# Optimization experiments

Measured on AMD Instinct MI355X. Metric: run time of the kernel, lower is better.

Reference implementation:

```python
import jax, jax.numpy as jnp
import numpy as np

N = 50000       # nodes
E = 800000      # directed edges (before self-loops)
IN = 128        # in_channels
H = 8           # heads
C = 32          # hidden_channels (per head)
OUT = 4         # out_channels
NS_ATT = 0.2    # PyG GATConv attention leaky-relu slope
NS_ACT = 0.01   # model activation leaky-relu slope
EPS = 1e-5      # BatchNorm eps


def setup_inputs() -> dict:
    key = jax.random.key(0)
    ks = jax.random.split(key, 18)
    s = 0.05
    return {
        "x": jax.random.normal(ks[0], (N, IN), jnp.float32),
        "edge_index": jax.random.randint(ks[1], (2, E), 0, N, dtype=jnp.int32),
        # layer 1: GATConv(IN -> C, heads=H, concat)
        "W1": jax.random.normal(ks[2], (IN, H * C), jnp.float32) * s,
        "as1": jax.random.normal(ks[3], (H, C), jnp.float32) * s,
        "ad1": jax.random.normal(ks[4], (H, C), jnp.float32) * s,
        "b1": jnp.zeros((H * C,), jnp.float32),
        "g1": jnp.ones((H * C,), jnp.float32),
        "be1": jnp.zeros((H * C,), jnp.float32),
        # middle layer: GATConv(H*C -> C, heads=H, concat) + BN + residual
        "W2": jax.random.normal(ks[5], (H * C, H * C), jnp.float32) * s,
        "as2": jax.random.normal(ks[6], (H, C), jnp.float32) * s,
        "ad2": jax.random.normal(ks[7], (H, C), jnp.float32) * s,
        "b2": jnp.zeros((H * C,), jnp.float32),
        "g2": jnp.ones((H * C,), jnp.float32),
        "be2": jnp.zeros((H * C,), jnp.float32),
        # final layer: GATConv(H*C -> OUT, heads=1, concat=False)
        "W3": jax.random.normal(ks[8], (H * C, OUT), jnp.float32) * s,
        "as3": jax.random.normal(ks[9], (1, OUT), jnp.float32) * s,
        "ad3": jax.random.normal(ks[10], (1, OUT), jnp.float32) * s,
        "b3": jnp.zeros((OUT,), jnp.float32),
    }


def _lrelu(x, slope):
    return jnp.where(x >= 0, x, slope * x)


def _gat_conv(x, src, dst, W, a_src, a_dst, bias, heads, ch, concat):
    # PyG GATConv: h = x @ W per head; edge logit = LReLU(a_src.h_j + a_dst.h_i)
    n = x.shape[0]
    h = (x @ W).reshape(n, heads, ch)                      # [N,H,C]
    al_s = jnp.sum(h * a_src, axis=-1)                     # [N,H]
    al_d = jnp.sum(h * a_dst, axis=-1)                     # [N,H]
    logits = _lrelu(al_s[src] + al_d[dst], NS_ATT)         # [E,H]
    # segment softmax over edges grouped by destination node
    m = jax.ops.segment_max(logits, dst, num_segments=n)   # [N,H]
    e = jnp.exp(logits - m[dst])
    denom = jax.ops.segment_sum(e, dst, num_segments=n)
    alpha = e / (denom[dst] + 1e-16)                       # [E,H]
    out = jax.ops.segment_sum(alpha[:, :, None] * h[src], dst, num_segments=n)  # [N,H,C]
    if concat:
        return out.reshape(n, heads * ch) + bias
    return out.mean(axis=1) + bias


def _bn(x, gamma, beta):
    mu = jnp.mean(x, axis=0)
    var = jnp.mean((x - mu) ** 2, axis=0)
    return (x - mu) * jax.lax.rsqrt(var + EPS) * gamma + beta


def reference(x, edge_index, W1, as1, ad1, b1, g1, be1,
              W2, as2, ad2, b2, g2, be2, W3, as3, ad3, b3):
    n = x.shape[0]
    loops = jnp.arange(n, dtype=edge_index.dtype)          # self-loops (PyG default)
    src = jnp.concatenate([edge_index[0], loops])
    dst = jnp.concatenate([edge_index[1], loops])
    h = _lrelu(_bn(_gat_conv(x, src, dst, W1, as1, ad1, b1, H, C, True), g1, be1), NS_ACT)
    residual = h
    h = _lrelu(_bn(_gat_conv(h, src, dst, W2, as2, ad2, b2, H, C, True), g2, be2), NS_ACT)
    h = h + residual
    return _gat_conv(h, src, dst, W3, as3, ad3, b3, 1, OUT, False)
```

## Files before the change

### kernel.cpp

```cpp
#include <hip/hip_runtime.h>

typedef __attribute__((ext_vector_type(8))) short bf16x8;
typedef __attribute__((ext_vector_type(4))) float f32x4;

__device__ __forceinline__ float lrelu(float x, float s) { return x >= 0.f ? x : s * x; }
__device__ __forceinline__ float b2f(unsigned short u) {
  union { unsigned int i; float f; } v; v.i = ((unsigned int)u) << 16; return v.f;
}
__device__ __forceinline__ float b2f_lo(unsigned int u) {
  union { unsigned int i; float f; } v; v.i = u << 16; return v.f;
}
__device__ __forceinline__ float b2f_hi(unsigned int u) {
  union { unsigned int i; float f; } v; v.i = u & 0xffff0000u; return v.f;
}
__device__ __forceinline__ unsigned short f2b(float f) {
  union { float f; unsigned int i; } v; v.f = f;
  unsigned int r = v.i + 0x7fffu + ((v.i >> 16) & 1u);
  return (unsigned short)(r >> 16);
}

__global__ __launch_bounds__(256) void k_hist(const int* __restrict__ dst, int e,
                                              int* __restrict__ cnt) {
  int i = blockIdx.x * 256 + threadIdx.x;
  if (i < e) atomicAdd(&cnt[dst[i]], 1);
}

__global__ __launch_bounds__(256) void k_bsum(const int* __restrict__ cnt,
                                              int* __restrict__ bsum, int n) {
  const int base = blockIdx.x * 1024;
  const int t = threadIdx.x;
  int s = 0;
#pragma unroll
  for (int i = 0; i < 4; ++i) {
    int idx = base + t + i * 256;
    if (idx < n) s += cnt[idx] + 1;
  }
#pragma unroll
  for (int off = 1; off < 64; off <<= 1) s += __shfl_xor(s, off);
  __shared__ int ws[4];
  const int lane = t & 63, w = t >> 6;
  if (lane == 0) ws[w] = s;
  __syncthreads();
  if (t == 0) bsum[blockIdx.x] = ws[0] + ws[1] + ws[2] + ws[3];
}

__global__ __launch_bounds__(64) void k_scanb(const int* __restrict__ bsum,
                                              int* __restrict__ boff,
                                              int* __restrict__ ptrN, int B) {
  const int lane = threadIdx.x;
  int v = lane < B ? bsum[lane] : 0;
  int incl = v;
#pragma unroll
  for (int off = 1; off < 64; off <<= 1) {
    int u = __shfl_up(incl, off);
    if (lane >= off) incl += u;
  }
  if (lane < B) boff[lane] = incl - v;
  if (lane == 63) *ptrN = incl;
}

__global__ __launch_bounds__(256) void k_scanl(const int* __restrict__ cnt,
                                               const int* __restrict__ boff,
                                               int* __restrict__ ptr,
                                               int* __restrict__ fill, int n) {
  __shared__ int ws[4];
  const int t = threadIdx.x;
  const int base = blockIdx.x * 1024 + t * 4;
  int v0 = base + 0 < n ? cnt[base + 0] + 1 : 0;
  int v1 = base + 1 < n ? cnt[base + 1] + 1 : 0;
  int v2 = base + 2 < n ? cnt[base + 2] + 1 : 0;
  int v3 = base + 3 < n ? cnt[base + 3] + 1 : 0;
  const int tsum = v0 + v1 + v2 + v3;
  const int lane = t & 63, w = t >> 6;
  int incl = tsum;
#pragma unroll
  for (int off = 1; off < 64; off <<= 1) {
    int u = __shfl_up(incl, off);
    if (lane >= off) incl += u;
  }
  if (lane == 63) ws[w] = incl;
  __syncthreads();
  int excl = boff[blockIdx.x] + incl - tsum;
  for (int i = 0; i < w; ++i) excl += ws[i];
  if (base + 0 < n) { ptr[base + 0] = excl; fill[base + 0] = excl; }
  excl += v0;
  if (base + 1 < n) { ptr[base + 1] = excl; fill[base + 1] = excl; }
  excl += v1;
  if (base + 2 < n) { ptr[base + 2] = excl; fill[base + 2] = excl; }
  excl += v2;
  if (base + 3 < n) { ptr[base + 3] = excl; fill[base + 3] = excl; }
}

__global__ __launch_bounds__(256) void k_scatter(const int* __restrict__ srce,
                                                 const int* __restrict__ dste,
                                                 int e, int n,
                                                 int* __restrict__ fill,
                                                 int* __restrict__ srcs) {
  int i = blockIdx.x * 256 + threadIdx.x;
  if (i < e) {
    int pos = atomicAdd(&fill[dste[i]], 1);
    srcs[pos] = srce[i];
  } else if (i < e + n) {
    int v = i - e;
    int pos = atomicAdd(&fill[v], 1);
    srcs[pos] = v;
  }
}

__global__ __launch_bounds__(256) void k_prep(const float* __restrict__ x,
                                              unsigned short* __restrict__ xb,
                                              const float* __restrict__ W1,
                                              unsigned short* __restrict__ w1t,
                                              const float* __restrict__ W2,
                                              unsigned short* __restrict__ w2t, int n4) {
  int i = blockIdx.x * 256 + threadIdx.x;
  if (i < n4) {
    float4 v = ((const float4*)x)[i];
    ushort4 o;
    o.x = f2b(v.x); o.y = f2b(v.y); o.z = f2b(v.z); o.w = f2b(v.w);
    ((ushort4*)xb)[i] = o;
    return;
  }
  i -= n4;
  if (i < 256 * 128) {
    int nn = i / 128, k = i - nn * 128;
    w1t[i] = f2b(W1[(size_t)k * 256 + nn]);
    return;
  }
  i -= 256 * 128;
  if (i < 256 * 256) {
    int nn = i / 256, k = i - nn * 256;
    w2t[i] = f2b(W2[(size_t)k * 256 + nn]);
  }
}

__global__ __launch_bounds__(256) void k_mfma(const unsigned short* __restrict__ A,
                                              const unsigned short* __restrict__ BT,
                                              unsigned short* __restrict__ C,
                                              int M, int Nn, int K) {
  __shared__ unsigned int Asu[128 * 20];
  __shared__ unsigned int Bsu[128 * 20];
  const int tid = threadIdx.x;
  const int bm = blockIdx.x * 128, bn = blockIdx.y * 128;
  const int w = tid >> 6, lane = tid & 63;
  const int wm = w >> 1, wn = w & 1;
  const int l16 = lane & 15, lg = lane >> 4;
  f32x4 acc[4][4] = {};
  for (int k0 = 0; k0 < K; k0 += 32) {
#pragma unroll
    for (int rep = 0; rep < 2; ++rep) {
      int ci = tid + rep * 256;
      int row = ci >> 2, cg = ci & 3;
      int ar = bm + row;
      ar = ar < M ? ar : M - 1;
      uint4 av = *(const uint4*)(A + (size_t)ar * K + k0 + cg * 8);
      *(uint4*)&Asu[row * 20 + cg * 4] = av;
      uint4 bv = *(const uint4*)(BT + (size_t)(bn + row) * K + k0 + cg * 8);
      *(uint4*)&Bsu[row * 20 + cg * 4] = bv;
    }
    __syncthreads();
    bf16x8 aF[4], bF[4];
#pragma unroll
    for (int mi = 0; mi < 4; ++mi)
      aF[mi] = *(const bf16x8*)&Asu[(wm * 64 + mi * 16 + l16) * 20 + lg * 4];
#pragma unroll
    for (int ni = 0; ni < 4; ++ni)
      bF[ni] = *(const bf16x8*)&Bsu[(wn * 64 + ni * 16 + l16) * 20 + lg * 4];
#pragma unroll
    for (int mi = 0; mi < 4; ++mi)
#pragma unroll
      for (int ni = 0; ni < 4; ++ni)
        acc[mi][ni] =
            __builtin_amdgcn_mfma_f32_16x16x32_bf16(aF[mi], bF[ni], acc[mi][ni], 0, 0, 0);
    __syncthreads();
  }
#pragma unroll
  for (int mi = 0; mi < 4; ++mi) {
#pragma unroll
    for (int r = 0; r < 4; ++r) {
      int grow = bm + wm * 64 + mi * 16 + lg * 4 + r;
      if (grow < M) {
#pragma unroll
        for (int ni = 0; ni < 4; ++ni) {
          int gcol = bn + wn * 64 + ni * 16 + l16;
          C[(size_t)grow * Nn + gcol] = f2b(acc[mi][ni][r]);
        }
      }
    }
  }
}

__global__ __launch_bounds__(256) void k_attn(const unsigned short* __restrict__ h,
                                              const float* __restrict__ as_,
                                              const float* __restrict__ ad_,
                                              float* __restrict__ als,
                                              float* __restrict__ ald, int n) {
  int wid = (blockIdx.x * 256 + threadIdx.x) >> 6;
  int lane = threadIdx.x & 63;
  if (wid >= n) return;
  ushort4 hv = *(const ushort4*)(h + (size_t)wid * 256 + lane * 4);
  float hx = b2f(hv.x), hy = b2f(hv.y), hz = b2f(hv.z), hw = b2f(hv.w);
  float4 av = *(const float4*)(as_ + lane * 4);
  float4 dv = *(const float4*)(ad_ + lane * 4);
  float ps = hx * av.x + hy * av.y + hz * av.z + hw * av.w;
  float pd = hx * dv.x + hy * dv.y + hz * dv.z + hw * dv.w;
  ps += __shfl_xor(ps, 1); pd += __shfl_xor(pd, 1);
  ps += __shfl_xor(ps, 2); pd += __shfl_xor(pd, 2);
  ps += __shfl_xor(ps, 4); pd += __shfl_xor(pd, 4);
  if ((lane & 7) == 0) {
    als[(size_t)wid * 8 + (lane >> 3)] = ps;
    ald[(size_t)wid * 8 + (lane >> 3)] = pd;
  }
}

__global__ __launch_bounds__(256) void k_agg(const unsigned short* __restrict__ h,
                                             const float* __restrict__ als,
                                             const float* __restrict__ ald,
                                             const int* __restrict__ ptr,
                                             const int* __restrict__ srcs,
                                             const float* __restrict__ bias,
                                             unsigned short* __restrict__ out, int n) {
  int wid = (blockIdx.x * 256 + threadIdx.x) >> 6;
  int lane = threadIdx.x & 63;
  if (wid >= n) return;
  const int beg = ptr[wid], end = ptr[wid + 1];
  const int L = lane & 31;
  const int half = lane >> 5;
  const int hh = L >> 2;
  const float adh = ald[(size_t)wid * 8 + hh];
  float s = 0.f;
  float a0 = 0.f, a1 = 0.f, a2 = 0.f, a3 = 0.f, a4 = 0.f, a5 = 0.f, a6 = 0.f, a7 = 0.f;
  int j = beg + half;
  int sN = j < end ? srcs[j] : 0;
  for (; j < end; j += 2) {
    int nj = j + 2;
    int sNn = nj < end ? srcs[nj] : 0;
    float lg = lrelu(als[(size_t)sN * 8 + hh] + adh, 0.2f);
    float wt = __expf(lg);
    s += wt;
    uint4 hv = *(const uint4*)(h + (size_t)sN * 256 + L * 8);
    a0 += wt * b2f_lo(hv.x); a1 += wt * b2f_hi(hv.x);
    a2 += wt * b2f_lo(hv.y); a3 += wt * b2f_hi(hv.y);
    a4 += wt * b2f_lo(hv.z); a5 += wt * b2f_hi(hv.z);
    a6 += wt * b2f_lo(hv.w); a7 += wt * b2f_hi(hv.w);
    sN = sNn;
  }
  a0 += __shfl_xor(a0, 32); a1 += __shfl_xor(a1, 32);
  a2 += __shfl_xor(a2, 32); a3 += __shfl_xor(a3, 32);
  a4 += __shfl_xor(a4, 32); a5 += __shfl_xor(a5, 32);
  a6 += __shfl_xor(a6, 32); a7 += __shfl_xor(a7, 32);
  s += __shfl_xor(s, 32);
  s += __shfl_xor(s, 1);
  s += __shfl_xor(s, 2);
  s *= 0.25f;
  const float inv = 1.f / (s + 1e-16f);
  if (half == 0) {
    const float4* bp = (const float4*)(bias + L * 8);
    float4 bv0 = bp[0], bv1 = bp[1];
    float o0 = a0 * inv + bv0.x, o1 = a1 * inv + bv0.y;
    float o2 = a2 * inv + bv0.z, o3 = a3 * inv + bv0.w;
    float o4 = a4 * inv + bv1.x, o5 = a5 * inv + bv1.y;
    float o6 = a6 * inv + bv1.z, o7 = a7 * inv + bv1.w;
    uint4 ov;
    ov.x = (unsigned int)f2b(o0) | ((unsigned int)f2b(o1) << 16);
    ov.y = (unsigned int)f2b(o2) | ((unsigned int)f2b(o3) << 16);
    ov.z = (unsigned int)f2b(o4) | ((unsigned int)f2b(o5) << 16);
    ov.w = (unsigned int)f2b(o6) | ((unsigned int)f2b(o7) << 16);
    *(uint4*)(out + (size_t)wid * 256 + L * 8) = ov;
  }
}

__global__ __launch_bounds__(256) void k_bnp1(const unsigned short* __restrict__ x,
                                              float* __restrict__ partial, int n) {
  const int t = threadIdx.x;
  const int q = t & 63;
  const int rsub = t >> 6;
  float s0 = 0, s1 = 0, s2 = 0, s3 = 0, q0 = 0, q1 = 0, q2 = 0, q3 = 0;
  for (int r = blockIdx.x * 4 + rsub; r < n; r += 1024) {
    ushort4 v = *(const ushort4*)(x + (size_t)r * 256 + q * 4);
    float f0 = b2f(v.x), f1 = b2f(v.y), f2 = b2f(v.z), f3 = b2f(v.w);
    s0 += f0; s1 += f1; s2 += f2; s3 += f3;
    q0 += f0 * f0; q1 += f1 * f1; q2 += f2 * f2; q3 += f3 * f3;
  }
  __shared__ float ls[4][512];
  ls[rsub][q * 4 + 0] = s0; ls[rsub][q * 4 + 1] = s1;
  ls[rsub][q * 4 + 2] = s2; ls[rsub][q * 4 + 3] = s3;
  ls[rsub][256 + q * 4 + 0] = q0; ls[rsub][256 + q * 4 + 1] = q1;
  ls[rsub][256 + q * 4 + 2] = q2; ls[rsub][256 + q * 4 + 3] = q3;
  __syncthreads();
  float a = ls[0][t] + ls[1][t] + ls[2][t] + ls[3][t];
  float b = ls[0][256 + t] + ls[1][256 + t] + ls[2][256 + t] + ls[3][256 + t];
  partial[blockIdx.x * 512 + t] = a;
  partial[blockIdx.x * 512 + 256 + t] = b;
}

__global__ __launch_bounds__(256) void k_bnp2(const float* __restrict__ partial,
                                              float* __restrict__ statsOut) {
  const int idx = blockIdx.x * 256 + threadIdx.x;
  float s = 0.f;
  for (int b = 0; b < 256; ++b) s += partial[b * 512 + idx];
  statsOut[idx] = s;
}

__global__ __launch_bounds__(256) void k_bnact(const unsigned short* __restrict__ x,
                                               const float* __restrict__ stats,
                                               const float* __restrict__ ga,
                                               const float* __restrict__ be,
                                               unsigned short* __restrict__ out, int n) {
  const float invn = 1.f / (float)n;
  const int tot4 = n * 64;
  for (int t = blockIdx.x * 256 + threadIdx.x; t < tot4; t += gridDim.x * 256) {
    int i0 = t * 4;
    int c = i0 & 255;
    ushort4 xu = *(const ushort4*)(x + i0);
    float4 sm = *(const float4*)(stats + c);
    float4 sq = *(const float4*)(stats + 256 + c);
    float4 gv = *(const float4*)(ga + c);
    float4 bev = *(const float4*)(be + c);
    float o0, o1, o2, o3, mu, var, sc;
    mu = sm.x * invn; var = sq.x * invn - mu * mu; sc = gv.x * rsqrtf(var + 1e-5f);
    o0 = (b2f(xu.x) - mu) * sc + bev.x; o0 = o0 >= 0.f ? o0 : 0.01f * o0;
    mu = sm.y * invn; var = sq.y * invn - mu * mu; sc = gv.y * rsqrtf(var + 1e-5f);
    o1 = (b2f(xu.y) - mu) * sc + bev.y; o1 = o1 >= 0.f ? o1 : 0.01f * o1;
    mu = sm.z * invn; var = sq.z * invn - mu * mu; sc = gv.z * rsqrtf(var + 1e-5f);
    o2 = (b2f(xu.z) - mu) * sc + bev.z; o2 = o2 >= 0.f ? o2 : 0.01f * o2;
    mu = sm.w * invn; var = sq.w * invn - mu * mu; sc = gv.w * rsqrtf(var + 1e-5f);
    o3 = (b2f(xu.w) - mu) * sc + bev.w; o3 = o3 >= 0.f ? o3 : 0.01f * o3;
    ushort4 ob;
    ob.x = f2b(o0); ob.y = f2b(o1); ob.z = f2b(o2); ob.w = f2b(o3);
    *(ushort4*)(out + i0) = ob;
  }
}

__global__ __launch_bounds__(256) void k_bnact3(const unsigned short* __restrict__ x,
                                                const float* __restrict__ stats,
                                                const float* __restrict__ ga,
                                                const float* __restrict__ be,
                                                const unsigned short* __restrict__ res,
                                                const float* __restrict__ W3,
                                                const float* __restrict__ as3,
                                                const float* __restrict__ ad3,
                                                float* __restrict__ h3,
                                                float* __restrict__ als3,
                                                float* __restrict__ ald3, int n) {
  const float invn = 1.f / (float)n;
  int wid = (blockIdx.x * 256 + threadIdx.x) >> 6;
  int lane = threadIdx.x & 63;
  if (wid >= n) return;
  const int c = lane * 4;
  ushort4 xu = *(const ushort4*)(x + (size_t)wid * 256 + c);
  ushort4 rv = *(const ushort4*)(res + (size_t)wid * 256 + c);
  float4 sm = *(const float4*)(stats + c);
  float4 sq = *(const float4*)(stats + 256 + c);
  float4 gv = *(const float4*)(ga + c);
  float4 bev = *(const float4*)(be + c);
  float o0, o1, o2, o3, mu, var, sc;
  mu = sm.x * invn; var = sq.x * invn - mu * mu; sc = gv.x * rsqrtf(var + 1e-5f);
  o0 = (b2f(xu.x) - mu) * sc + bev.x; o0 = (o0 >= 0.f ? o0 : 0.01f * o0) + b2f(rv.x);
  mu = sm.y * invn; var = sq.y * invn - mu * mu; sc = gv.y * rsqrtf(var + 1e-5f);
  o1 = (b2f(xu.y) - mu) * sc + bev.y; o1 = (o1 >= 0.f ? o1 : 0.01f * o1) + b2f(rv.y);
  mu = sm.z * invn; var = sq.z * invn - mu * mu; sc = gv.z * rsqrtf(var + 1e-5f);
  o2 = (b2f(xu.z) - mu) * sc + bev.z; o2 = (o2 >= 0.f ? o2 : 0.01f * o2) + b2f(rv.z);
  mu = sm.w * invn; var = sq.w * invn - mu * mu; sc = gv.w * rsqrtf(var + 1e-5f);
  o3 = (b2f(xu.w) - mu) * sc + bev.w; o3 = (o3 >= 0.f ? o3 : 0.01f * o3) + b2f(rv.w);
  const float4* Wp = (const float4*)W3 + lane * 4;
  float4 w0 = Wp[0], w1 = Wp[1], w2 = Wp[2], w3 = Wp[3];
  float a0 = o0 * w0.x + o1 * w1.x + o2 * w2.x + o3 * w3.x;
  float a1 = o0 * w0.y + o1 * w1.y + o2 * w2.y + o3 * w3.y;
  float a2 = o0 * w0.z + o1 * w1.z + o2 * w2.z + o3 * w3.z;
  float a3 = o0 * w0.w + o1 * w1.w + o2 * w2.w + o3 * w3.w;
#pragma unroll
  for (int off = 1; off < 64; off <<= 1) {
    a0 += __shfl_xor(a0, off);
    a1 += __shfl_xor(a1, off);
    a2 += __shfl_xor(a2, off);
    a3 += __shfl_xor(a3, off);
  }
  if (lane == 0) {
    *(float4*)(h3 + (size_t)wid * 4) = make_float4(a0, a1, a2, a3);
    als3[wid] = a0 * as3[0] + a1 * as3[1] + a2 * as3[2] + a3 * as3[3];
    ald3[wid] = a0 * ad3[0] + a1 * ad3[1] + a2 * ad3[2] + a3 * ad3[3];
  }
}

__global__ __launch_bounds__(256) void k_agg3(const float* __restrict__ h3,
                                              const float* __restrict__ als3,
                                              const float* __restrict__ ald3,
                                              const int* __restrict__ ptr,
                                              const int* __restrict__ srcs,
                                              const float* __restrict__ b3,
                                              float* __restrict__ out, int n) {
  int wid = (blockIdx.x * 256 + threadIdx.x) >> 6;
  int lane = threadIdx.x & 63;
  if (wid >= n) return;
  const int beg = ptr[wid], end = ptr[wid + 1];
  const float aldh = ald3[wid];
  float s = 0.f, a0 = 0.f, a1 = 0.f, a2 = 0.f, a3 = 0.f;
  for (int j = beg + lane; j < end; j += 64) {
    int sN = srcs[j];
    float wgt = __expf(lrelu(als3[sN] + aldh, 0.2f));
    s += wgt;
    float4 hv = *(const float4*)(h3 + (size_t)sN * 4);
    a0 += wgt * hv.x;
    a1 += wgt * hv.y;
    a2 += wgt * hv.z;
    a3 += wgt * hv.w;
  }
#pragma unroll
  for (int off = 1; off < 64; off <<= 1) {
    s += __shfl_xor(s, off);
    a0 += __shfl_xor(a0, off);
    a1 += __shfl_xor(a1, off);
    a2 += __shfl_xor(a2, off);
    a3 += __shfl_xor(a3, off);
  }
  if (lane == 0) {
    float inv = 1.f / (s + 1e-16f);
    out[(size_t)wid * 4 + 0] = a0 * inv + b3[0];
    out[(size_t)wid * 4 + 1] = a1 * inv + b3[1];
    out[(size_t)wid * 4 + 2] = a2 * inv + b3[2];
    out[(size_t)wid * 4 + 3] = a3 * inv + b3[3];
  }
}

extern "C" void kernel_launch(void* const* d_in, const int* in_sizes, int n_in,
                              void* d_out, int out_size, void* d_ws, size_t ws_size,
                              hipStream_t stream) {
  const float* x   = (const float*)d_in[0];
  const int*   ei  = (const int*)d_in[1];
  const float* W1  = (const float*)d_in[2];
  const float* as1 = (const float*)d_in[3];
  const float* ad1 = (const float*)d_in[4];
  const float* b1  = (const float*)d_in[5];
  const float* ga1 = (const float*)d_in[6];
  const float* be1 = (const float*)d_in[7];
  const float* W2  = (const float*)d_in[8];
  const float* as2 = (const float*)d_in[9];
  const float* ad2 = (const float*)d_in[10];
  const float* b2  = (const float*)d_in[11];
  const float* ga2 = (const float*)d_in[12];
  const float* be2 = (const float*)d_in[13];
  const float* W3  = (const float*)d_in[14];
  const float* as3 = (const float*)d_in[15];
  const float* ad3 = (const float*)d_in[16];
  const float* b3  = (const float*)d_in[17];

  const int N = in_sizes[0] / 128;
  const int E = in_sizes[1] / 2;
  const int ET = E + N;
  float* out = (float*)d_out;

  char* w = (char*)d_ws;
  auto alloc = [&](size_t bytes) -> void* {
    void* p = (void*)w;
    w += (bytes + 255) & ~(size_t)255;
    return p;
  };
  int* ptr              = (int*)alloc((size_t)(N + 1) * 4);
  int* fill             = (int*)alloc((size_t)N * 4);
  int* cnt              = (int*)alloc((size_t)N * 4);
  int* bsum             = (int*)alloc(64 * 4);
  int* boff             = (int*)alloc(64 * 4);
  int* srcs             = (int*)alloc((size_t)ET * 4);
  unsigned short* hbuf  = (unsigned short*)alloc((size_t)N * 256 * 2);
  unsigned short* aggb  = (unsigned short*)alloc((size_t)N * 256 * 2);
  unsigned short* a1b   = (unsigned short*)alloc((size_t)N * 256 * 2);
  unsigned short* xb    = (unsigned short*)alloc((size_t)N * 128 * 2);
  unsigned short* w1t   = (unsigned short*)alloc(256 * 128 * 2);
  unsigned short* w2t   = (unsigned short*)alloc(256 * 256 * 2);
  float* als            = (float*)alloc((size_t)N * 8 * 4);
  float* ald            = (float*)alloc((size_t)N * 8 * 4);
  float* h3             = (float*)alloc((size_t)N * 4 * 4);
  float* als3           = (float*)alloc((size_t)N * 4);
  float* ald3           = (float*)alloc((size_t)N * 4);
  float* partial        = (float*)alloc(256 * 512 * 4);
  float* stats          = (float*)alloc(1024 * 4);

  const int* esrc = ei;
  const int* edst = ei + E;

  hipMemsetAsync(cnt, 0, (size_t)N * 4, stream);

  const int B = (N + 1023) / 1024;
  k_hist<<<(E + 255) / 256, 256, 0, stream>>>(edst, E, cnt);
  k_bsum<<<B, 256, 0, stream>>>(cnt, bsum, N);
  k_scanb<<<1, 64, 0, stream>>>(bsum, boff, ptr + N, B);
  k_scanl<<<B, 256, 0, stream>>>(cnt, boff, ptr, fill, N);
  k_scatter<<<(ET + 255) / 256, 256, 0, stream>>>(esrc, edst, E, N, fill, srcs);

  const int n4 = N * 32;
  const int prep_tot = n4 + 256 * 128 + 256 * 256;
  k_prep<<<(prep_tot + 255) / 256, 256, 0, stream>>>(x, xb, W1, w1t, W2, w2t, n4);

  const dim3 gemm_grid((N + 127) / 128, 2);
  const int wblocks = (N + 3) / 4;

  k_mfma<<<gemm_grid, 256, 0, stream>>>(xb, w1t, hbuf, N, 256, 128);
  k_attn<<<wblocks, 256, 0, stream>>>(hbuf, as1, ad1, als, ald, N);
  k_agg<<<wblocks, 256, 0, stream>>>(hbuf, als, ald, ptr, srcs, b1, aggb, N);
  k_bnp1<<<256, 256, 0, stream>>>(aggb, partial, N);
  k_bnp2<<<2, 256, 0, stream>>>(partial, stats);
  k_bnact<<<1024, 256, 0, stream>>>(aggb, stats, ga1, be1, a1b, N);

  k_mfma<<<gemm_grid, 256, 0, stream>>>(a1b, w2t, hbuf, N, 256, 256);
  k_attn<<<wblocks, 256, 0, stream>>>(hbuf, as2, ad2, als, ald, N);
  k_agg<<<wblocks, 256, 0, stream>>>(hbuf, als, ald, ptr, srcs, b2, aggb, N);
  k_bnp1<<<256, 256, 0, stream>>>(aggb, partial, N);
  k_bnp2<<<2, 256, 0, stream>>>(partial, stats + 512);
  k_bnact3<<<wblocks, 256, 0, stream>>>(aggb, stats + 512, ga2, be2, a1b,
                                        W3, as3, ad3, h3, als3, ald3, N);

  k_agg3<<<wblocks, 256, 0, stream>>>(h3, als3, ald3, ptr, srcs, b3, out, N);
}
```

Measured before the change: 420.2 us.

## Fuse attention logits into GEMM epilogue and widen edge parallelism in aggregation

Computes the per-head source/destination attention dot products directly from the fp32 MFMA accumulators in the GEMM epilogue, removing the separate k_attn kernel and its reread of h. The aggregation kernel now processes four edges per wave concurrently, with each lane handling 16 channels, to increase memory-level parallelism on the gathered rows. Attention scores now come from unrounded fp32 values rather than bf16 h, which slightly changes numerics. The GEMM epilogue gains extra shuffles and register pressure.

Measured after the change: 405.1 us. -3.6%, faster.

```diff
diff --git a/kernel.cpp b/kernel.cpp
--- a/kernel.cpp
+++ b/kernel.cpp
@@ -137,6 +137,10 @@
 __global__ __launch_bounds__(256) void k_mfma(const unsigned short* __restrict__ A,
                                               const unsigned short* __restrict__ BT,
                                               unsigned short* __restrict__ C,
+                                              const float* __restrict__ as_,
+                                              const float* __restrict__ ad_,
+                                              float* __restrict__ als,
+                                              float* __restrict__ ald,
                                               int M, int Nn, int K) {
   __shared__ unsigned int Asu[128 * 20];
   __shared__ unsigned int Bsu[128 * 20];
@@ -174,42 +178,43 @@
             __builtin_amdgcn_mfma_f32_16x16x32_bf16(aF[mi], bF[ni], acc[mi][ni], 0, 0, 0);
     __syncthreads();
   }
+  float asv[4], adv[4];
+#pragma unroll
+  for (int ni = 0; ni < 4; ++ni) {
+    int gcol = bn + wn * 64 + ni * 16 + l16;
+    asv[ni] = as_[gcol];
+    adv[ni] = ad_[gcol];
+  }
+  const int hb = (bn >> 5) + wn * 2;
 #pragma unroll
   for (int mi = 0; mi < 4; ++mi) {
 #pragma unroll
     for (int r = 0; r < 4; ++r) {
       int grow = bm + wm * 64 + mi * 16 + lg * 4 + r;
-      if (grow < M) {
+      bool ok = grow < M;
+      if (ok) {
 #pragma unroll
         for (int ni = 0; ni < 4; ++ni) {
           int gcol = bn + wn * 64 + ni * 16 + l16;
           C[(size_t)grow * Nn + gcol] = f2b(acc[mi][ni][r]);
         }
       }
+      float ps0 = acc[mi][0][r] * asv[0] + acc[mi][1][r] * asv[1];
+      float ps1 = acc[mi][2][r] * asv[2] + acc[mi][3][r] * asv[3];
+      float pd0 = acc[mi][0][r] * adv[0] + acc[mi][1][r] * adv[1];
+      float pd1 = acc[mi][2][r] * adv[2] + acc[mi][3][r] * adv[3];
+#pragma unroll
+      for (int off = 1; off < 16; off <<= 1) {
+        ps0 += __shfl_xor(ps0, off);
+        ps1 += __shfl_xor(ps1, off);
+        pd0 += __shfl_xor(pd0, off);
+        pd1 += __shfl_xor(pd1, off);
+      }
+      if (ok && l16 == 0) {
+        *(float2*)(als + (size_t)grow * 8 + hb) = make_float2(ps0, ps1);
+        *(float2*)(ald + (size_t)grow * 8 + hb) = make_float2(pd0, pd1);
+      }
     }
-  }
-}
-
-__global__ __launch_bounds__(256) void k_attn(const unsigned short* __restrict__ h,
-                                              const float* __restrict__ as_,
-                                              const float* __restrict__ ad_,
-                                              float* __restrict__ als,
-                                              float* __restrict__ ald, int n) {
-  int wid = (blockIdx.x * 256 + threadIdx.x) >> 6;
-  int lane = threadIdx.x & 63;
-  if (wid >= n) return;
-  ushort4 hv = *(const ushort4*)(h + (size_t)wid * 256 + lane * 4);
-  float hx = b2f(hv.x), hy = b2f(hv.y), hz = b2f(hv.z), hw = b2f(hv.w);
-  float4 av = *(const float4*)(as_ + lane * 4);
-  float4 dv = *(const float4*)(ad_ + lane * 4);
-  float ps = hx * av.x + hy * av.y + hz * av.z + hw * av.w;
-  float pd = hx * dv.x + hy * dv.y + hz * dv.z + hw * dv.w;
-  ps += __shfl_xor(ps, 1); pd += __shfl_xor(pd, 1);
-  ps += __shfl_xor(ps, 2); pd += __shfl_xor(pd, 2);
-  ps += __shfl_xor(ps, 4); pd += __shfl_xor(pd, 4);
-  if ((lane & 7) == 0) {
-    als[(size_t)wid * 8 + (lane >> 3)] = ps;
-    ald[(size_t)wid * 8 + (lane >> 3)] = pd;
   }
 }
 
@@ -224,49 +229,67 @@
   int lane = threadIdx.x & 63;
   if (wid >= n) return;
   const int beg = ptr[wid], end = ptr[wid + 1];
-  const int L = lane & 31;
-  const int half = lane >> 5;
-  const int hh = L >> 2;
+  const int L = lane & 15;
+  const int e = lane >> 4;
+  const int hh = L >> 1;
   const float adh = ald[(size_t)wid * 8 + hh];
   float s = 0.f;
-  float a0 = 0.f, a1 = 0.f, a2 = 0.f, a3 = 0.f, a4 = 0.f, a5 = 0.f, a6 = 0.f, a7 = 0.f;
-  int j = beg + half;
+  float a0 = 0, a1 = 0, a2 = 0, a3 = 0, a4 = 0, a5 = 0, a6 = 0, a7 = 0;
+  float a8 = 0, a9 = 0, aA = 0, aB = 0, aC = 0, aD = 0, aE = 0, aF = 0;
+  int j = beg + e;
   int sN = j < end ? srcs[j] : 0;
-  for (; j < end; j += 2) {
-    int nj = j + 2;
+  for (; j < end; j += 4) {
+    int nj = j + 4;
     int sNn = nj < end ? srcs[nj] : 0;
     float lg = lrelu(als[(size_t)sN * 8 + hh] + adh, 0.2f);
     float wt = __expf(lg);
     s += wt;
-    uint4 hv = *(const uint4*)(h + (size_t)sN * 256 + L * 8);
-    a0 += wt * b2f_lo(hv.x); a1 += wt * b2f_hi(hv.x);
-    a2 += wt * b2f_lo(hv.y); a3 += wt * b2f_hi(hv.y);
-    a4 += wt * b2f_lo(hv.z); a5 += wt * b2f_hi(hv.z);
-    a6 += wt * b2f_lo(hv.w); a7 += wt * b2f_hi(hv.w);
+    const uint4* hp = (const uint4*)(h + (size_t)sN * 256 + L * 16);
+    uint4 h0 = hp[0];
+    uint4 h1 = hp[1];
+    a0 += wt * b2f_lo(h0.x); a1 += wt * b2f_hi(h0.x);
+    a2 += wt * b2f_lo(h0.y); a3 += wt * b2f_hi(h0.y);
+    a4 += wt * b2f_lo(h0.z); a5 += wt * b2f_hi(h0.z);
+    a6 += wt * b2f_lo(h0.w); a7 += wt * b2f_hi(h0.w);
+    a8 += wt * b2f_lo(h1.x); a9 += wt * b2f_hi(h1.x);
+    aA += wt * b2f_lo(h1.y); aB += wt * b2f_hi(h1.y);
+    aC += wt * b2f_lo(h1.z); aD += wt * b2f_hi(h1.z);
+    aE += wt * b2f_lo(h1.w); aF += wt * b2f_hi(h1.w);
     sN = sNn;
   }
-  a0 += __shfl_xor(a0, 32); a1 += __shfl_xor(a1, 32);
-  a2 += __shfl_xor(a2, 32); a3 += __shfl_xor(a3, 32);
-  a4 += __shfl_xor(a4, 32); a5 += __shfl_xor(a5, 32);
-  a6 += __shfl_xor(a6, 32); a7 += __shfl_xor(a7, 32);
-  s += __shfl_xor(s, 32);
-  s += __shfl_xor(s, 1);
-  s += __shfl_xor(s, 2);
-  s *= 0.25f;
+  a0 += __shfl_xor(a0, 16); a0 += __shfl_xor(a0, 32);
+  a1 += __shfl_xor(a1, 16); a1 += __shfl_xor(a1, 32);
+  a2 += __shfl_xor(a2, 16); a2 += __shfl_xor(a2, 32);
+  a3 += __shfl_xor(a3, 16); a3 += __shfl_xor(a3, 32);
+  a4 += __shfl_xor(a4, 16); a4 += __shfl_xor(a4, 32);
+  a5 += __shfl_xor(a5, 16); a5 += __shfl_xor(a5, 32);
+  a6 += __shfl_xor(a6, 16); a6 += __shfl_xor(a6, 32);
+  a7 += __shfl_xor(a7, 16); a7 += __shfl_xor(a7, 32);
+  a8 += __shfl_xor(a8, 16); a8 += __shfl_xor(a8, 32);
+  a9 += __shfl_xor(a9, 16); a9 += __shfl_xor(a9, 32);
+  aA += __shfl_xor(aA, 16); aA += __shfl_xor(aA, 32);
+  aB += __shfl_xor(aB, 16); aB += __shfl_xor(aB, 32);
+  aC += __shfl_xor(aC, 16); aC += __shfl_xor(aC, 32);
+  aD += __shfl_xor(aD, 16); aD += __shfl_xor(aD, 32);
+  aE += __shfl_xor(aE, 16); aE += __shfl_xor(aE, 32);
+  aF += __shfl_xor(aF, 16); aF += __shfl_xor(aF, 32);
+  s += __shfl_xor(s, 16); s += __shfl_xor(s, 32);
   const float inv = 1.f / (s + 1e-16f);
-  if (half == 0) {
-    const float4* bp = (const float4*)(bias + L * 8);
-    float4 bv0 = bp[0], bv1 = bp[1];
-    float o0 = a0 * inv + bv0.x, o1 = a1 * inv + bv0.y;
-    float o2 = a2 * inv + bv0.z, o3 = a3 * inv + bv0.w;
-    float o4 = a4 * inv + bv1.x, o5 = a5 * inv + bv1.y;
-    float o6 = a6 * inv + bv1.z, o7 = a7 * inv + bv1.w;
-    uint4 ov;
-    ov.x = (unsigned int)f2b(o0) | ((unsigned int)f2b(o1) << 16);
-    ov.y = (unsigned int)f2b(o2) | ((unsigned int)f2b(o3) << 16);
-    ov.z = (unsigned int)f2b(o4) | ((unsigned int)f2b(o5) << 16);
-    ov.w = (unsigned int)f2b(o6) | ((unsigned int)f2b(o7) << 16);
-    *(uint4*)(out + (size_t)wid * 256 + L * 8) = ov;
+  if (e == 0) {
+    const float4* bp = (const float4*)(bias + L * 16);
+    float4 b0 = bp[0], b1 = bp[1], b2 = bp[2], b3 = bp[3];
+    uint4 o0, o1;
+    o0.x = (unsigned int)f2b(a0 * inv + b0.x) | ((unsigned int)f2b(a1 * inv + b0.y) << 16);
+    o0.y = (unsigned int)f2b(a2 * inv + b0.z) | ((unsigned int)f2b(a3 * inv + b0.w) << 16);
+    o0.z = (unsigned int)f2b(a4 * inv + b1.x) | ((unsigned int)f2b(a5 * inv + b1.y) << 16);
+    o0.w = (unsigned int)f2b(a6 * inv + b1.z) | ((unsigned int)f2b(a7 * inv + b1.w) << 16);
+    o1.x = (unsigned int)f2b(a8 * inv + b2.x) | ((unsigned int)f2b(a9 * inv + b2.y) << 16);
+    o1.y = (unsigned int)f2b(aA * inv + b2.z) | ((unsigned int)f2b(aB * inv + b2.w) << 16);
+    o1.z = (unsigned int)f2b(aC * inv + b3.x) | ((unsigned int)f2b(aD * inv + b3.y) << 16);
+    o1.w = (unsigned int)f2b(aE * inv + b3.z) | ((unsigned int)f2b(aF * inv + b3.w) << 16);
+    uint4* op = (uint4*)(out + (size_t)wid * 256 + L * 16);
+    op[0] = o0;
+    op[1] = o1;
   }
 }
 
@@ -495,15 +518,13 @@
   const dim3 gemm_grid((N + 127) / 128, 2);
   const int wblocks = (N + 3) / 4;
 
-  k_mfma<<<gemm_grid, 256, 0, stream>>>(xb, w1t, hbuf, N, 256, 128);
-  k_attn<<<wblocks, 256, 0, stream>>>(hbuf, as1, ad1, als, ald, N);
+  k_mfma<<<gemm_grid, 256, 0, stream>>>(xb, w1t, hbuf, as1, ad1, als, ald, N, 256, 128);
   k_agg<<<wblocks, 256, 0, stream>>>(hbuf, als, ald, ptr, srcs, b1, aggb, N);
   k_bnp1<<<256, 256, 0, stream>>>(aggb, partial, N);
   k_bnp2<<<2, 256, 0, stream>>>(partial, stats);
   k_bnact<<<1024, 256, 0, stream>>>(aggb, stats, ga1, be1, a1b, N);
 
-  k_mfma<<<gemm_grid, 256, 0, stream>>>(a1b, w2t, hbuf, N, 256, 256);
-  k_attn<<<wblocks, 256, 0, stream>>>(hbuf, as2, ad2, als, ald, N);
+  k_mfma<<<gemm_grid, 256, 0, stream>>>(a1b, w2t, hbuf, as2, ad2, als, ald, N, 256, 256);
   k_agg<<<wblocks, 256, 0, stream>>>(hbuf, als, ald, ptr, srcs, b2, aggb, N);
   k_bnp1<<<256, 256, 0, stream>>>(aggb, partial, N);
   k_bnp2<<<2, 256, 0, stream>>>(partial, stats + 512);
```
